# Kernel tuning notes

Hardware: AMD Instinct MI355X
Metric: run time of the kernel (lower is better)

The kernel has to match this reference:

```python
import jax, jax.numpy as jnp
import numpy as np


def setup_inputs() -> dict:
    key = jax.random.key(0)
    k1, k2, k3 = jax.random.split(key, 3)
    B, H, S, D = 2, 16, 2048, 64
    q = jax.random.normal(k1, (B, H, S, D), dtype=jnp.float32)
    k = jax.random.normal(k2, (B, H, S, D), dtype=jnp.float32)
    v = jax.random.normal(k3, (B, H, S, D), dtype=jnp.float32)
    return {"q": q, "k": k, "v": v}


def reference(q, k, v):
    # q,k,v: [B,H,S,D]; causal attention with 1/sqrt(D) scaling, fp32 softmax.
    scale = 1.0 / (q.shape[-1] ** 0.5)
    scores = jnp.einsum('bhqd,bhkd->bhqk', q * scale, k)  # [B,H,S,S]
    S = scores.shape[-1]
    causal_mask = jnp.triu(jnp.ones((S, S), dtype=bool), k=1)
    scores = jnp.where(causal_mask, -jnp.inf, scores)
    attn = jax.nn.softmax(scores.astype(jnp.float32), axis=-1).astype(q.dtype)
    output = jnp.einsum('bhqk,bhkd->bhqd', attn, v)
    # Module also returns an all-zeros attn_weights placeholder of shape [B,H,S,S]
    attn_weights = jnp.zeros(scores.shape, dtype=q.dtype)
    return (output, attn_weights)
```

## Files before the change

kernel.cpp:

```cpp
#include <hip/hip_runtime.h>


typedef __bf16 bf16x8 __attribute__((ext_vector_type(8)));
typedef float f32x4 __attribute__((ext_vector_type(4)));

#define LOG2E 1.44269504088896340736f

__device__ __forceinline__ unsigned short f2bf(float f) {
  unsigned int u = __float_as_uint(f);
  u += 0x7fffu + ((u >> 16) & 1u);
  return (unsigned short)(u >> 16);
}

union U8 { unsigned short u[8]; bf16x8 v; };

constexpr int Sdim = 2048, Ddim = 64, BHn = 32;
constexpr int BM = 64, BN = 64;
constexpr int QTiles = Sdim / BM;
constexpr int LDK = 72;
constexpr int OUT0 = BHn * Sdim * Ddim;
constexpr int ZF4_PER_BLOCK = 32768;

__global__ __launch_bounds__(256, 2)
void flash_causal_kernel(const float* __restrict__ Q, const float* __restrict__ K,
                         const float* __restrict__ V, float* __restrict__ out) {
  __shared__ unsigned short Klds[BN * LDK];
  __shared__ unsigned short Vlds[Ddim * LDK];
  __shared__ unsigned short Plds[4][16 * LDK];

  const int tid  = threadIdx.x;
  const int wave = tid >> 6;
  const int lane = tid & 63;
  const int quad = lane >> 4;
  const int l15  = lane & 15;

  const int bh = blockIdx.x & (BHn - 1);
  const int qt = (QTiles - 1) - (int)(blockIdx.x >> 5);

  const int base  = bh * Sdim * Ddim;
  const int qrow0 = qt * BM + wave * 16;

  bf16x8 aq[2];
  {
    const float* qp = Q + base + (qrow0 + l15) * Ddim + quad * 8;
    #pragma unroll
    for (int s = 0; s < 2; ++s) {
      float4 a = *(const float4*)(qp + 32 * s);
      float4 b = *(const float4*)(qp + 32 * s + 4);
      U8 u;
      u.u[0] = f2bf(a.x * 0.125f); u.u[1] = f2bf(a.y * 0.125f);
      u.u[2] = f2bf(a.z * 0.125f); u.u[3] = f2bf(a.w * 0.125f);
      u.u[4] = f2bf(b.x * 0.125f); u.u[5] = f2bf(b.y * 0.125f);
      u.u[6] = f2bf(b.z * 0.125f); u.u[7] = f2bf(b.w * 0.125f);
      aq[s] = u.v;
    }
  }

  f32x4 ot[4];
  #pragma unroll
  for (int t = 0; t < 4; ++t) ot[t] = (f32x4){0.f, 0.f, 0.f, 0.f};
  float mrun[4], lrun[4];
  #pragma unroll
  for (int r = 0; r < 4; ++r) { mrun[r] = -__builtin_inff(); lrun[r] = 0.f; }

  const float4* kg4 = (const float4*)(K + base);
  const float4* vg4 = (const float4*)(V + base);

  for (int j = 0; j <= qt; ++j) {
    const float4* kp = kg4 + j * 1024;
    const float4* vp = vg4 + j * 1024;
    #pragma unroll
    for (int rr = 0; rr < 4; ++rr) {
      int lin = rr * 256 + tid;
      int row = lin >> 4;
      int c4  = (lin & 15) << 2;
      float4 fk = kp[lin];
      float4 fv = vp[lin];
      unsigned int k01 = (unsigned int)f2bf(fk.x) | ((unsigned int)f2bf(fk.y) << 16);
      unsigned int k23 = (unsigned int)f2bf(fk.z) | ((unsigned int)f2bf(fk.w) << 16);
      uint2 t2; t2.x = k01; t2.y = k23;
      *(uint2*)&Klds[row * LDK + c4] = t2;
      Vlds[(c4 + 0) * LDK + row] = f2bf(fv.x);
      Vlds[(c4 + 1) * LDK + row] = f2bf(fv.y);
      Vlds[(c4 + 2) * LDK + row] = f2bf(fv.z);
      Vlds[(c4 + 3) * LDK + row] = f2bf(fv.w);
    }
    __syncthreads();

    f32x4 sc[4];
    #pragma unroll
    for (int t = 0; t < 4; ++t) sc[t] = (f32x4){0.f, 0.f, 0.f, 0.f};
    #pragma unroll
    for (int s = 0; s < 2; ++s) {
      #pragma unroll
      for (int t = 0; t < 4; ++t) {
        bf16x8 bk = *(const bf16x8*)&Klds[(16 * t + l15) * LDK + 32 * s + quad * 8];
        sc[t] = __builtin_amdgcn_mfma_f32_16x16x32_bf16(aq[s], bk, sc[t], 0, 0, 0);
      }
    }

    if (j == qt) {
      #pragma unroll
      for (int t = 0; t < 4; ++t)
        #pragma unroll
        for (int r = 0; r < 4; ++r)
          if (16 * t + l15 > wave * 16 + quad * 4 + r) sc[t][r] = -__builtin_inff();
    }

    float mx[4];
    #pragma unroll
    for (int r = 0; r < 4; ++r) {
      float m0 = fmaxf(fmaxf(sc[0][r], sc[1][r]), fmaxf(sc[2][r], sc[3][r]));
      #pragma unroll
      for (int off = 1; off < 16; off <<= 1) m0 = fmaxf(m0, __shfl_xor(m0, off));
      mx[r] = m0;
    }
    float alpha[4], msc[4];
    #pragma unroll
    for (int r = 0; r < 4; ++r) {
      float mn = fmaxf(mrun[r], mx[r]);
      alpha[r] = __builtin_amdgcn_exp2f((mrun[r] - mn) * LOG2E);
      msc[r]   = mn * LOG2E;
      mrun[r]  = mn;
    }
    float rs[4] = {0.f, 0.f, 0.f, 0.f};
    #pragma unroll
    for (int t = 0; t < 4; ++t)
      #pragma unroll
      for (int r = 0; r < 4; ++r) {
        float p = __builtin_amdgcn_exp2f(fmaf(sc[t][r], LOG2E, -msc[r]));
        sc[t][r] = p;
        rs[r] += p;
      }
    #pragma unroll
    for (int r = 0; r < 4; ++r) {
      #pragma unroll
      for (int off = 1; off < 16; off <<= 1) rs[r] += __shfl_xor(rs[r], off);
      lrun[r] = lrun[r] * alpha[r] + rs[r];
    }
    #pragma unroll
    for (int t = 0; t < 4; ++t)
      #pragma unroll
      for (int r = 0; r < 4; ++r) ot[t][r] *= alpha[r];

    #pragma unroll
    for (int t = 0; t < 4; ++t)
      #pragma unroll
      for (int r = 0; r < 4; ++r)
        Plds[wave][(quad * 4 + r) * LDK + 16 * t + l15] = f2bf(sc[t][r]);

    #pragma unroll
    for (int s = 0; s < 2; ++s) {
      bf16x8 ap = *(const bf16x8*)&Plds[wave][l15 * LDK + 32 * s + quad * 8];
      #pragma unroll
      for (int t = 0; t < 4; ++t) {
        bf16x8 bv = *(const bf16x8*)&Vlds[(16 * t + l15) * LDK + 32 * s + quad * 8];
        ot[t] = __builtin_amdgcn_mfma_f32_16x16x32_bf16(ap, bv, ot[t], 0, 0, 0);
      }
    }
    __syncthreads();
  }

  #pragma unroll
  for (int r = 0; r < 4; ++r) {
    float inv = 1.0f / lrun[r];
    float* orow = out + base + (qrow0 + quad * 4 + r) * Ddim + l15;
    #pragma unroll
    for (int t = 0; t < 4; ++t) orow[16 * t] = ot[t][r] * inv;
  }

  {
    f32x4 z4 = (f32x4){0.f, 0.f, 0.f, 0.f};
    f32x4* zp = (f32x4*)(out + OUT0) + (size_t)blockIdx.x * ZF4_PER_BLOCK + tid;
    #pragma unroll 8
    for (int i = 0; i < ZF4_PER_BLOCK / 256; ++i)
      __builtin_nontemporal_store(z4, zp + i * 256);
  }
}

extern "C" void kernel_launch(void* const* d_in, const int* in_sizes, int n_in,
                              void* d_out, int out_size, void* d_ws, size_t ws_size,
                              hipStream_t stream) {
  const float* q = (const float*)d_in[0];
  const float* k = (const float*)d_in[1];
  const float* v = (const float*)d_in[2];
  float* out = (float*)d_out;
  dim3 grid(BHn * QTiles);
  flash_causal_kernel<<<grid, dim3(256), 0, stream>>>(q, k, v, out);
}
```

Baseline: 639.6 us.

## Prefetch K/V tiles into registers, transpose MFMA layout, rebalance zero-fill work

The K/V global loads for the next tile are now issued into registers before the current tile's compute, so memory latency overlaps with the MFMAs. The MFMA operands are swapped so each lane owns one query row: row max and sum need only two cross-lane shuffles, P is written to LDS with packed 8-byte stores, and the output is stored as float4. The zero-fill of the attention-weights buffer is redistributed so that blocks with little causal work (large g) zero more memory, which balances per-block runtime. The cost is extra registers for the prefetch buffers, which may reduce occupancy.

```diff
diff --git a/kernel.cpp b/kernel.cpp
--- a/kernel.cpp
+++ b/kernel.cpp
@@ -15,16 +15,14 @@
 union U8 { unsigned short u[8]; bf16x8 v; };
 
 constexpr int Sdim = 2048, Ddim = 64, BHn = 32;
-constexpr int BM = 64, BN = 64;
-constexpr int QTiles = Sdim / BM;
+constexpr int QTiles = Sdim / 64;
 constexpr int LDK = 72;
 constexpr int OUT0 = BHn * Sdim * Ddim;
-constexpr int ZF4_PER_BLOCK = 32768;
 
 __global__ __launch_bounds__(256, 2)
 void flash_causal_kernel(const float* __restrict__ Q, const float* __restrict__ K,
                          const float* __restrict__ V, float* __restrict__ out) {
-  __shared__ unsigned short Klds[BN * LDK];
+  __shared__ unsigned short Klds[64 * LDK];
   __shared__ unsigned short Vlds[Ddim * LDK];
   __shared__ unsigned short Plds[4][16 * LDK];
 
@@ -35,10 +33,11 @@
   const int l15  = lane & 15;
 
   const int bh = blockIdx.x & (BHn - 1);
-  const int qt = (QTiles - 1) - (int)(blockIdx.x >> 5);
+  const int g  = (int)(blockIdx.x >> 5);
+  const int qt = (QTiles - 1) - g;
 
   const int base  = bh * Sdim * Ddim;
-  const int qrow0 = qt * BM + wave * 16;
+  const int qrow0 = qt * 64 + wave * 16;
 
   bf16x8 aq[2];
   {
@@ -59,34 +58,46 @@
   f32x4 ot[4];
   #pragma unroll
   for (int t = 0; t < 4; ++t) ot[t] = (f32x4){0.f, 0.f, 0.f, 0.f};
-  float mrun[4], lrun[4];
-  #pragma unroll
-  for (int r = 0; r < 4; ++r) { mrun[r] = -__builtin_inff(); lrun[r] = 0.f; }
+  float mrun = -__builtin_inff(), lrun = 0.f;
 
   const float4* kg4 = (const float4*)(K + base);
   const float4* vg4 = (const float4*)(V + base);
 
+  float4 kf[4], vf[4];
+  #pragma unroll
+  for (int i = 0; i < 4; ++i) {
+    kf[i] = kg4[i * 256 + tid];
+    vf[i] = vg4[i * 256 + tid];
+  }
+
   for (int j = 0; j <= qt; ++j) {
-    const float4* kp = kg4 + j * 1024;
-    const float4* vp = vg4 + j * 1024;
-    #pragma unroll
-    for (int rr = 0; rr < 4; ++rr) {
-      int lin = rr * 256 + tid;
+    __syncthreads();
+    #pragma unroll
+    for (int i = 0; i < 4; ++i) {
+      int lin = i * 256 + tid;
       int row = lin >> 4;
       int c4  = (lin & 15) << 2;
-      float4 fk = kp[lin];
-      float4 fv = vp[lin];
-      unsigned int k01 = (unsigned int)f2bf(fk.x) | ((unsigned int)f2bf(fk.y) << 16);
-      unsigned int k23 = (unsigned int)f2bf(fk.z) | ((unsigned int)f2bf(fk.w) << 16);
+      unsigned int k01 = (unsigned int)f2bf(kf[i].x) | ((unsigned int)f2bf(kf[i].y) << 16);
+      unsigned int k23 = (unsigned int)f2bf(kf[i].z) | ((unsigned int)f2bf(kf[i].w) << 16);
       uint2 t2; t2.x = k01; t2.y = k23;
       *(uint2*)&Klds[row * LDK + c4] = t2;
-      Vlds[(c4 + 0) * LDK + row] = f2bf(fv.x);
-      Vlds[(c4 + 1) * LDK + row] = f2bf(fv.y);
-      Vlds[(c4 + 2) * LDK + row] = f2bf(fv.z);
-      Vlds[(c4 + 3) * LDK + row] = f2bf(fv.w);
+      Vlds[(c4 + 0) * LDK + row] = f2bf(vf[i].x);
+      Vlds[(c4 + 1) * LDK + row] = f2bf(vf[i].y);
+      Vlds[(c4 + 2) * LDK + row] = f2bf(vf[i].z);
+      Vlds[(c4 + 3) * LDK + row] = f2bf(vf[i].w);
     }
     __syncthreads();
 
+    if (j < qt) {
+      const float4* kp = kg4 + (j + 1) * 1024;
+      const float4* vp = vg4 + (j + 1) * 1024;
+      #pragma unroll
+      for (int i = 0; i < 4; ++i) {
+        kf[i] = kp[i * 256 + tid];
+        vf[i] = vp[i * 256 + tid];
+      }
+    }
+
     f32x4 sc[4];
     #pragma unroll
     for (int t = 0; t < 4; ++t) sc[t] = (f32x4){0.f, 0.f, 0.f, 0.f};
@@ -94,87 +105,87 @@
     for (int s = 0; s < 2; ++s) {
       #pragma unroll
       for (int t = 0; t < 4; ++t) {
-        bf16x8 bk = *(const bf16x8*)&Klds[(16 * t + l15) * LDK + 32 * s + quad * 8];
-        sc[t] = __builtin_amdgcn_mfma_f32_16x16x32_bf16(aq[s], bk, sc[t], 0, 0, 0);
+        bf16x8 ka = *(const bf16x8*)&Klds[(16 * t + l15) * LDK + 32 * s + quad * 8];
+        sc[t] = __builtin_amdgcn_mfma_f32_16x16x32_bf16(ka, aq[s], sc[t], 0, 0, 0);
       }
     }
 
     if (j == qt) {
+      const int qml = wave * 16 + l15;
       #pragma unroll
       for (int t = 0; t < 4; ++t)
         #pragma unroll
         for (int r = 0; r < 4; ++r)
-          if (16 * t + l15 > wave * 16 + quad * 4 + r) sc[t][r] = -__builtin_inff();
-    }
-
-    float mx[4];
-    #pragma unroll
-    for (int r = 0; r < 4; ++r) {
-      float m0 = fmaxf(fmaxf(sc[0][r], sc[1][r]), fmaxf(sc[2][r], sc[3][r]));
-      #pragma unroll
-      for (int off = 1; off < 16; off <<= 1) m0 = fmaxf(m0, __shfl_xor(m0, off));
-      mx[r] = m0;
-    }
-    float alpha[4], msc[4];
-    #pragma unroll
-    for (int r = 0; r < 4; ++r) {
-      float mn = fmaxf(mrun[r], mx[r]);
-      alpha[r] = __builtin_amdgcn_exp2f((mrun[r] - mn) * LOG2E);
-      msc[r]   = mn * LOG2E;
-      mrun[r]  = mn;
-    }
-    float rs[4] = {0.f, 0.f, 0.f, 0.f};
+          if (16 * t + 4 * quad + r > qml) sc[t][r] = -__builtin_inff();
+    }
+
+    float mx = sc[0][0];
     #pragma unroll
     for (int t = 0; t < 4; ++t)
       #pragma unroll
+      for (int r = 0; r < 4; ++r) mx = fmaxf(mx, sc[t][r]);
+    mx = fmaxf(mx, __shfl_xor(mx, 16));
+    mx = fmaxf(mx, __shfl_xor(mx, 32));
+    float mn    = fmaxf(mrun, mx);
+    float alpha = __builtin_amdgcn_exp2f((mrun - mn) * LOG2E);
+    float msc   = mn * LOG2E;
+    mrun = mn;
+    float rs = 0.f;
+    #pragma unroll
+    for (int t = 0; t < 4; ++t)
+      #pragma unroll
       for (int r = 0; r < 4; ++r) {
-        float p = __builtin_amdgcn_exp2f(fmaf(sc[t][r], LOG2E, -msc[r]));
+        float p = __builtin_amdgcn_exp2f(fmaf(sc[t][r], LOG2E, -msc));
         sc[t][r] = p;
-        rs[r] += p;
-      }
-    #pragma unroll
-    for (int r = 0; r < 4; ++r) {
-      #pragma unroll
-      for (int off = 1; off < 16; off <<= 1) rs[r] += __shfl_xor(rs[r], off);
-      lrun[r] = lrun[r] * alpha[r] + rs[r];
-    }
+        rs += p;
+      }
+    rs += __shfl_xor(rs, 16);
+    rs += __shfl_xor(rs, 32);
+    lrun = lrun * alpha + rs;
     #pragma unroll
     for (int t = 0; t < 4; ++t)
       #pragma unroll
-      for (int r = 0; r < 4; ++r) ot[t][r] *= alpha[r];
-
-    #pragma unroll
-    for (int t = 0; t < 4; ++t)
-      #pragma unroll
-      for (int r = 0; r < 4; ++r)
-        Plds[wave][(quad * 4 + r) * LDK + 16 * t + l15] = f2bf(sc[t][r]);
+      for (int r = 0; r < 4; ++r) ot[t][r] *= alpha;
+
+    #pragma unroll
+    for (int t = 0; t < 4; ++t) {
+      uint2 pw;
+      pw.x = (unsigned int)f2bf(sc[t][0]) | ((unsigned int)f2bf(sc[t][1]) << 16);
+      pw.y = (unsigned int)f2bf(sc[t][2]) | ((unsigned int)f2bf(sc[t][3]) << 16);
+      *(uint2*)&Plds[wave][l15 * LDK + 16 * t + 4 * quad] = pw;
+    }
 
     #pragma unroll
     for (int s = 0; s < 2; ++s) {
-      bf16x8 ap = *(const bf16x8*)&Plds[wave][l15 * LDK + 32 * s + quad * 8];
+      bf16x8 pb = *(const bf16x8*)&Plds[wave][l15 * LDK + 32 * s + quad * 8];
       #pragma unroll
       for (int t = 0; t < 4; ++t) {
-        bf16x8 bv = *(const bf16x8*)&Vlds[(16 * t + l15) * LDK + 32 * s + quad * 8];
-        ot[t] = __builtin_amdgcn_mfma_f32_16x16x32_bf16(ap, bv, ot[t], 0, 0, 0);
-      }
-    }
-    __syncthreads();
-  }
-
-  #pragma unroll
-  for (int r = 0; r < 4; ++r) {
-    float inv = 1.0f / lrun[r];
-    float* orow = out + base + (qrow0 + quad * 4 + r) * Ddim + l15;
-    #pragma unroll
-    for (int t = 0; t < 4; ++t) orow[16 * t] = ot[t][r] * inv;
+        bf16x8 va = *(const bf16x8*)&Vlds[(16 * t + l15) * LDK + 32 * s + quad * 8];
+        ot[t] = __builtin_amdgcn_mfma_f32_16x16x32_bf16(va, pb, ot[t], 0, 0, 0);
+      }
+    }
   }
 
   {
+    float inv = 1.0f / lrun;
+    float* orow = out + base + (qrow0 + l15) * Ddim + 4 * quad;
+    #pragma unroll
+    for (int t = 0; t < 4; ++t) {
+      f32x4 o4;
+      o4.x = ot[t][0] * inv; o4.y = ot[t][1] * inv;
+      o4.z = ot[t][2] * inv; o4.w = ot[t][3] * inv;
+      *(f32x4*)(orow + 16 * t) = o4;
+    }
+  }
+
+  {
+    const int w = 2 * g + 1;
+    const size_t start_f4 = (size_t)1024 * (32 * (size_t)(g * g) + (size_t)bh * w);
+    const size_t count_f4 = (size_t)1024 * w;
     f32x4 z4 = (f32x4){0.f, 0.f, 0.f, 0.f};
-    f32x4* zp = (f32x4*)(out + OUT0) + (size_t)blockIdx.x * ZF4_PER_BLOCK + tid;
-    #pragma unroll 8
-    for (int i = 0; i < ZF4_PER_BLOCK / 256; ++i)
-      __builtin_nontemporal_store(z4, zp + i * 256);
+    f32x4* zp = (f32x4*)(out + OUT0) + start_f4;
+    for (size_t i = tid; i < count_f4; i += 256)
+      __builtin_nontemporal_store(z4, zp + i);
   }
 }
 
```

New measurement: 621.1 us. -2.9%, faster.
